# Performance work log

Measured on AMD Instinct MI355X. Metric: run time of the kernel, lower is better.

The kernel has to match this reference:

```python
import jax, jax.numpy as jnp
import numpy as np
import math

NHID = 32
FEAT_SIZE = 32
FEAT_SIZE_LIST = [16, 32, 32, 32]
SEQ_LEN = len(FEAT_SIZE_LIST)   # 4
N_EDGE_LABELS = 3
NLAYERS = 2
N_GRAPHS = 64
FINAL = SEQ_LEN * NHID          # 128


def _pos_enc(max_len, dim):
    pe = np.zeros((max_len, dim), dtype=np.float32)
    pos = np.arange(max_len, dtype=np.float32)[:, None]
    div = np.exp(np.arange(0, dim, 2, dtype=np.float32) * (-math.log(10000.0) / dim))
    pe[:, 0::2] = np.sin(pos * div)
    pe[:, 1::2] = np.cos(pos * div)
    return jnp.asarray(pe)


def _feature_attention(x, wqkv, w1, b1, w2, b2):
    # x: [N, S*NHID] -> attention over the S feature 'tokens' per node
    N, D = x.shape
    S = D // NHID
    xr = x.reshape(N, S, NHID)
    qkv = jnp.einsum('nsf,fh->nsh', xr, wqkv)          # [N,S,3*NHID]
    q, k, v = jnp.split(qkv, 3, axis=-1)
    att = jax.nn.softmax(jnp.einsum('nsh,nth->nst', q, k) / jnp.sqrt(jnp.asarray(NHID, x.dtype)), axis=-1)
    y = jnp.einsum('nst,nth->nsh', att, v)             # [N,S,NHID]
    y = y + (jax.nn.relu(y @ w1 + b1) @ w2 + b2)       # residual FFN
    return y.reshape(N, -1)


def setup_inputs() -> dict:
    key = jax.random.key(0)
    ks = jax.random.split(key, 16)
    N = 100000
    E = 800000
    inp = {
        'x': jax.random.normal(ks[0], (N, 112), dtype=jnp.float32),
        'edge_index0': jax.random.randint(ks[1], (2, E), 0, N),
        'edge_index1': jax.random.randint(ks[2], (2, E), 0, N),
        'edge_index2': jax.random.randint(ks[3], (2, E), 0, N),
        'batch': jnp.sort(jax.random.randint(ks[4], (N,), 0, N_GRAPHS)),
    }
    s = 0.05
    # FeatureLinear encoder (bias-free)
    inp['W_emb'] = jax.random.normal(ks[5], (FEAT_SIZE, NHID), dtype=jnp.float32) * s
    # Per layer: [root, conv0, conv1, conv2] FeatureAttention params, stacked
    A = 1 + N_EDGE_LABELS
    inp['qkv'] = jax.random.normal(ks[6], (NLAYERS, A, NHID, 3 * NHID), dtype=jnp.float32) * s
    inp['ffn_w1'] = jax.random.normal(ks[7], (NLAYERS, A, NHID, NHID), dtype=jnp.float32) * s
    inp['ffn_b1'] = jnp.zeros((NLAYERS, A, NHID), dtype=jnp.float32)
    inp['ffn_w2'] = jax.random.normal(ks[8], (NLAYERS, A, NHID, NHID), dtype=jnp.float32) * s
    inp['ffn_b2'] = jnp.zeros((NLAYERS, A, NHID), dtype=jnp.float32)
    # Heuristic decoder MLP: 128 -> 128 -> 1
    inp['mlp_w1'] = jax.random.normal(ks[9], (FINAL, FINAL), dtype=jnp.float32) * s
    inp['mlp_b1'] = jnp.zeros((FINAL,), dtype=jnp.float32)
    inp['mlp_w2'] = jax.random.normal(ks[10], (FINAL, 1), dtype=jnp.float32) * s
    inp['mlp_b2'] = jnp.zeros((1,), dtype=jnp.float32)
    return inp


def reference(x, edge_index0, edge_index1, edge_index2, batch,
              W_emb, qkv, ffn_w1, ffn_b1, ffn_w2, ffn_b2,
              mlp_w1, mlp_b1, mlp_w2, mlp_b2):
    N = x.shape[0]
    edge_indices = [edge_index0, edge_index1, edge_index2]

    # padding: split by feat_size_list, right-pad each chunk to FEAT_SIZE
    offs = np.cumsum(FEAT_SIZE_LIST)[:-1].tolist()
    chunks = jnp.split(x, offs, axis=1)
    padded = [jnp.pad(c, ((0, 0), (0, FEAT_SIZE - c.shape[1]))) for c in chunks]
    h = jnp.concatenate(padded, axis=1)                       # [N, SEQ_LEN*FEAT_SIZE]

    # sinusoidal positional encoding over the SEQ_LEN feature tokens
    pe = _pos_enc(10, FEAT_SIZE)[:SEQ_LEN]                    # [SEQ_LEN, FEAT_SIZE]
    h = (h.reshape(N, SEQ_LEN, FEAT_SIZE) + pe[None]).reshape(N, -1)

    # FeatureLinear encoder: per-token linear FEAT_SIZE -> NHID
    h = jnp.einsum('nsf,fh->nsh', h.reshape(N, SEQ_LEN, FEAT_SIZE), W_emb).reshape(N, -1)

    # RGNN layers: root attention + per-edge-label attention->scatter-sum
    for l in range(NLAYERS):
        x_out = _feature_attention(h, qkv[l, 0], ffn_w1[l, 0], ffn_b1[l, 0], ffn_w2[l, 0], ffn_b2[l, 0])
        for e in range(N_EDGE_LABELS):
            a = e + 1
            xt = _feature_attention(h, qkv[l, a], ffn_w1[l, a], ffn_b1[l, a], ffn_w2[l, a], ffn_b2[l, a])
            src, dst = edge_indices[e][0], edge_indices[e][1]
            x_out = x_out + jax.ops.segment_sum(xt[src], dst, num_segments=N)
        h = jax.nn.relu(x_out)

    # global mean pool over graphs
    sums = jax.ops.segment_sum(h, batch, num_segments=N_GRAPHS)
    cnts = jax.ops.segment_sum(jnp.ones((N,), h.dtype), batch, num_segments=N_GRAPHS)
    g = sums / jnp.maximum(cnts, 1.0)[:, None]                # [G, FINAL]

    # heuristic decoder
    out = jax.nn.relu(g @ mlp_w1 + mlp_b1) @ mlp_w2 + mlp_b2  # [G, 1]
    return out.squeeze(1)                                     # [G]
```

## Files before the change

kernel.cpp:

```cpp
#include <hip/hip_runtime.h>
#include <hip/hip_bf16.h>
#include <cstdint>
#include <cstddef>


typedef __attribute__((ext_vector_type(8))) short bf16x8;
typedef __attribute__((ext_vector_type(4))) float f32x4;
typedef __attribute__((ext_vector_type(2))) float f32x2;

#if defined(__has_builtin)
#if __has_builtin(__builtin_amdgcn_cvt_pk_fp8_f32) && __has_builtin(__builtin_amdgcn_cvt_pk_f32_fp8)
#define HW_FP8 1
#endif
#if __has_builtin(__builtin_amdgcn_cvt_pk_bf16_f32)
#define HW_PKBF16 1
#endif
#endif

__device__ inline short f2bf(float f) {
    union { float f; unsigned u; } v; v.f = f;
    unsigned r = (v.u + 0x7FFFu + ((v.u >> 16) & 1u)) >> 16;
    return (short)r;
}
__device__ inline float bf2f(unsigned short b) {
    union { unsigned u; float f; } v; v.u = ((unsigned)b) << 16;
    return v.f;
}
#ifdef HW_PKBF16
typedef __attribute__((ext_vector_type(2))) __bf16 bf16x2_t;
__device__ inline unsigned pk2(float a, float b) {
    union { bf16x2_t v; unsigned u; } c;
    c.v = __builtin_amdgcn_cvt_pk_bf16_f32(a, b);
    return c.u;
}
#else
__device__ inline unsigned pk2(float a, float b) {
    unsigned ua = __float_as_uint(a) + 0x8000u;
    unsigned ub = __float_as_uint(b) + 0x8000u;
    return __builtin_amdgcn_perm(ub, ua, 0x07060302u);
}
#endif

#ifndef HW_FP8
__device__ inline unsigned char f2fp8_sw(float f) {
    unsigned s = (__float_as_uint(f) >> 31) & 1u;
    float a = fminf(fabsf(f), 448.f);
    unsigned char bits;
    if (a < 0.015625f) {
        bits = (unsigned char)__float2int_rn(a * 512.f);
    } else {
        int e; float m = frexpf(a, &e);
        int mf = __float2int_rn(m * 16.f);
        if (mf == 16) { mf = 8; e += 1; }
        int ef = e - 1 + 7;
        if (ef > 15) { ef = 15; mf = 14; }
        bits = (unsigned char)((ef << 3) | (mf & 7));
    }
    return (unsigned char)((s << 7) | bits);
}
__device__ inline float fp82f_sw(unsigned b) {
    int s = (b >> 7) & 1, e = (b >> 3) & 15, m = b & 7;
    float v = e ? ldexpf((float)(8 + m), e - 10) : ldexpf((float)m, -9);
    return s ? -v : v;
}
#endif

__device__ inline unsigned pk4fp8(float v0, float v1, float v2, float v3) {
#ifdef HW_FP8
    int w = __builtin_amdgcn_cvt_pk_fp8_f32(v0, v1, 0, false);
    w = __builtin_amdgcn_cvt_pk_fp8_f32(v2, v3, w, true);
    return (unsigned)w;
#else
    return (unsigned)f2fp8_sw(v0) | ((unsigned)f2fp8_sw(v1) << 8) |
           ((unsigned)f2fp8_sw(v2) << 16) | ((unsigned)f2fp8_sw(v3) << 24);
#endif
}
__device__ inline float2 up2fp8(unsigned short raw) {
#ifdef HW_FP8
    f32x2 f = __builtin_amdgcn_cvt_pk_f32_fp8((int)(unsigned)raw, false);
    return make_float2(f[0], f[1]);
#else
    return make_float2(fp82f_sw(raw & 0xffu), fp82f_sw((raw >> 8) & 0xffu));
#endif
}

__device__ inline void acc8(float* a, uint2 v) {
#ifdef HW_FP8
    f32x2 f0 = __builtin_amdgcn_cvt_pk_f32_fp8((int)v.x, false);
    f32x2 f1 = __builtin_amdgcn_cvt_pk_f32_fp8((int)v.x, true);
    f32x2 f2 = __builtin_amdgcn_cvt_pk_f32_fp8((int)v.y, false);
    f32x2 f3 = __builtin_amdgcn_cvt_pk_f32_fp8((int)v.y, true);
    a[0] += f0[0]; a[1] += f0[1]; a[2] += f1[0]; a[3] += f1[1];
    a[4] += f2[0]; a[5] += f2[1]; a[6] += f3[0]; a[7] += f3[1];
#else
    unsigned b0 = v.x, b1 = v.y;
#pragma unroll
    for (int j = 0; j < 4; ++j) a[j]     += fp82f_sw((b0 >> (8 * j)) & 0xffu);
#pragma unroll
    for (int j = 0; j < 4; ++j) a[4 + j] += fp82f_sw((b1 >> (8 * j)) & 0xffu);
#endif
}

__global__ __launch_bounds__(64) void wprep_kernel(
    const float* __restrict__ qkv, const float* __restrict__ fw1,
    const float* __restrict__ fw2, const float* __restrict__ Wemb,
    unsigned short* __restrict__ wpack, float* __restrict__ pwc,
    int* __restrict__ bcnt, int* __restrict__ gres,
    float* __restrict__ gsum, float* __restrict__ gcnt)
{
    const int pi = blockIdx.x;
    const int lane = threadIdx.x;
    const int gid = pi * 64 + lane;
    for (int i = gid; i < 256; i += 512) { bcnt[i] = 0; gres[i] = 0; }
    for (int i = gid; i < 64 * 128; i += 512) gsum[i] = 0.f;
    if (gid < 64) gcnt[gid] = 0.f;

    const int q = lane >> 4, m = lane & 15;
    const float* Wq = qkv + (size_t)pi * 32 * 96;
    const float* W1 = fw1 + (size_t)pi * 32 * 32;
    const float* W2 = fw2 + (size_t)pi * 32 * 32;
    unsigned short* dst = wpack + (size_t)pi * 10 * 64 * 8;
#pragma unroll
    for (int ci = 0; ci < 6; ++ci)
#pragma unroll
        for (int j = 0; j < 8; ++j)
            dst[(ci * 64 + lane) * 8 + j] =
                (unsigned short)f2bf(Wq[(q * 8 + j) * 96 + ci * 16 + m]);
#pragma unroll
    for (int t = 0; t < 2; ++t)
#pragma unroll
        for (int j = 0; j < 8; ++j) {
            dst[((6 + t) * 64 + lane) * 8 + j] =
                (unsigned short)f2bf(W1[(q * 8 + j) * 32 + t * 16 + m]);
            dst[((8 + t) * 64 + lane) * 8 + j] =
                (unsigned short)f2bf(W2[(q * 8 + j) * 32 + t * 16 + m]);
        }

    if (pi == 0) {
        const int c = lane & 31;
        for (int ts = lane >> 5; ts < 4; ts += 2) {
            float accp = 0.f;
            for (int f = 0; f < 32; ++f) {
                float div = __expf(-(float)(f & ~1) * (logf(10000.0f) / 32.0f));
                float ang = (float)ts * div;
                float pv = (f & 1) ? cosf(ang) : sinf(ang);
                accp += pv * Wemb[f * 32 + c];
            }
            pwc[ts * 32 + c] = accp;
        }
    }
}

__global__ __launch_bounds__(256) void enc_kernel(
    const float* __restrict__ x, const float* __restrict__ Wemb,
    const float* __restrict__ pwc, unsigned short* __restrict__ h, int N)
{
    __shared__ float sx[64 * 116];
    const int t = threadIdx.x;
    const int nbase = blockIdx.x * 64;

    {
        const float4* xg = (const float4*)x;
        const size_t g4base = ((size_t)nbase * 112) >> 2;
        const size_t lim4 = ((size_t)N * 112) >> 2;
#pragma unroll
        for (int rep = 0; rep < 7; ++rep) {
            int i = t + rep * 256;
            float4 v = make_float4(0.f, 0.f, 0.f, 0.f);
            if (g4base + (size_t)i < lim4) v = xg[g4base + i];
            int row = i / 28;
            int col4 = i - row * 28;
            *(float4*)&sx[row * 116 + col4 * 4] = v;
        }
    }
    __syncthreads();

    const int nl = t >> 2, ts = t & 3;
    const int node = nbase + nl;
    const int offs_[4] = {0, 16, 48, 80};
    const int nv_[4] = {4, 8, 8, 8};
    const int off = offs_[ts];
    const int nv = nv_[ts];

    float xr[32];
#pragma unroll
    for (int j = 0; j < 8; ++j) {
        float4 v = make_float4(0.f, 0.f, 0.f, 0.f);
        if (j < nv) v = *(const float4*)&sx[nl * 116 + off + 4 * j];
        *(float4*)&xr[4 * j] = v;
    }

    float acc[32];
    {
        const float4* pw4 = (const float4*)(pwc + ts * 32);
#pragma unroll
        for (int j = 0; j < 8; ++j) *(float4*)&acc[4 * j] = pw4[j];
    }

#pragma unroll
    for (int f = 0; f < 32; ++f) {
        float xv = xr[f];
#pragma unroll
        for (int c = 0; c < 32; ++c)
            acc[c] = fmaf(xv, Wemb[f * 32 + c], acc[c]);
    }

    if (node < N) {
        unsigned rp[16];
#pragma unroll
        for (int j = 0; j < 16; ++j) rp[j] = pk2(acc[2 * j], acc[2 * j + 1]);
        unsigned short* hp = h + (size_t)node * 128 + ts * 32;
#pragma unroll
        for (int j = 0; j < 4; ++j)
            ((uint4*)hp)[j] = make_uint4(rp[4 * j], rp[4 * j + 1],
                                         rp[4 * j + 2], rp[4 * j + 3]);
    }
}

#define ATT_WAVES 4
#define WLDS 5376

__global__ __launch_bounds__(256, 3) void attn4_kernel(
    const unsigned short* __restrict__ in,
    unsigned short* __restrict__ outR, unsigned char* __restrict__ out3,
    const unsigned short* __restrict__ wpack,
    const float* __restrict__ fb1, const float* __restrict__ fb2,
    int pibase, int N)
{
    __shared__ char smem[ATT_WAVES * 2 * WLDS];
    const int lane = threadIdx.x & 63;
    const int wave = threadIdx.x >> 6;
    const int q = lane >> 4;
    const int m = lane & 15;

    char* wb0 = smem + wave * (2 * WLDS);

#pragma unroll
    for (int u = 0; u < 2; ++u) {
        int* p32 = (int*)(wb0 + u * WLDS + 4096);
        for (int i = lane; i < 320; i += 64) p32[i] = 0;
    }

    const f32x4 zf = {0.f, 0.f, 0.f, 0.f};
    const int pi = pibase + wave;
    unsigned char* out8 = out3 + (size_t)(wave - 1) * N * 128;

    bf16x8 wqkv[6], w1f[2], w2f[2];
    float b1r[2][4], b2r[2][4];
    {
        const unsigned short* wp = wpack + ((size_t)pi * 10 * 64 + lane) * 8;
#pragma unroll
        for (int ci = 0; ci < 6; ++ci)
            wqkv[ci] = *(const bf16x8*)(wp + ci * 64 * 8);
#pragma unroll
        for (int t = 0; t < 2; ++t) {
            w1f[t] = *(const bf16x8*)(wp + (6 + t) * 64 * 8);
            w2f[t] = *(const bf16x8*)(wp + (8 + t) * 64 * 8);
#pragma unroll
            for (int r = 0; r < 4; ++r) {
                b1r[t][r] = fb1[pi * 32 + 16 * t + q * 4 + r];
                b2r[t][r] = fb2[pi * 32 + 16 * t + q * 4 + r];
            }
        }
    }

    const int nsuper = (N + 7) >> 3;
    for (int stile = blockIdx.x; stile < nsuper; stile += gridDim.x) {
        const int n0 = stile * 8;

        bf16x8 ax[2];
#pragma unroll
        for (int u = 0; u < 2; ++u) {
            bf16x8 a = {0, 0, 0, 0, 0, 0, 0, 0};
            int nm = n0 + 4 * u + (m >> 2);
            if (nm < N)
                a = *(const bf16x8*)(in + (size_t)(n0 + 4 * u) * 128 + m * 32 + q * 8);
            ax[u] = a;
        }

#pragma unroll
        for (int u = 0; u < 2; ++u) {
            char* wbu = wb0 + u * WLDS;
            short* Qb = (short*)(wbu);
            short* Kb = (short*)(wbu + 1280);
            short* VT = (short*)(wbu + 2560);
            short* Pb = (short*)(wbu + 4096);

            f32x4 aQ[2], aK[2], aV[2];
#pragma unroll
            for (int t = 0; t < 2; ++t) {
                aQ[t] = __builtin_amdgcn_mfma_f32_16x16x32_bf16(wqkv[t],     ax[u], zf, 0, 0, 0);
                aK[t] = __builtin_amdgcn_mfma_f32_16x16x32_bf16(wqkv[2 + t], ax[u], zf, 0, 0, 0);
                aV[t] = __builtin_amdgcn_mfma_f32_16x16x32_bf16(ax[u], wqkv[4 + t], zf, 0, 0, 0);
            }
#pragma unroll
            for (int t = 0; t < 2; ++t) {
                uint2 dq, dk, dv;
                dq.x = pk2(aQ[t][0], aQ[t][1]); dq.y = pk2(aQ[t][2], aQ[t][3]);
                dk.x = pk2(aK[t][0], aK[t][1]); dk.y = pk2(aK[t][2], aK[t][3]);
                dv.x = pk2(aV[t][0], aV[t][1]); dv.y = pk2(aV[t][2], aV[t][3]);
                *(uint2*)(Qb + m * 40 + 16 * t + q * 4) = dq;
                *(uint2*)(Kb + m * 40 + 16 * t + q * 4) = dk;
                *(uint2*)(VT + (16 * t + m) * 24 + q * 4) = dv;
            }

            bf16x8 aKf = *(const bf16x8*)(Kb + m * 40 + q * 8);
            bf16x8 bQf = *(const bf16x8*)(Qb + m * 40 + q * 8);
            f32x4 st = __builtin_amdgcn_mfma_f32_16x16x32_bf16(aKf, bQf, zf, 0, 0, 0);

            float v0 = st[0] * 0.1767766952966369f;
            float v1 = st[1] * 0.1767766952966369f;
            float v2 = st[2] * 0.1767766952966369f;
            float v3 = st[3] * 0.1767766952966369f;
            float mx = fmaxf(fmaxf(v0, v1), fmaxf(v2, v3));
            float e0 = __expf(v0 - mx), e1 = __expf(v1 - mx);
            float e2 = __expf(v2 - mx), e3 = __expf(v3 - mx);
            float inv = 1.0f / (e0 + e1 + e2 + e3);
            if (q == (m >> 2)) {
                uint2 dp;
                dp.x = pk2(e0 * inv, e1 * inv);
                dp.y = pk2(e2 * inv, e3 * inv);
                *(uint2*)(Pb + m * 40 + q * 4) = dp;
            }

            f32x4 y[2];
#pragma unroll
            for (int t = 0; t < 2; ++t) {
                bf16x8 aVf = {0, 0, 0, 0, 0, 0, 0, 0};
                bf16x8 bPf = {0, 0, 0, 0, 0, 0, 0, 0};
                if (q < 2) {
                    aVf = *(const bf16x8*)(VT + (16 * t + m) * 24 + q * 8);
                    bPf = *(const bf16x8*)(Pb + m * 40 + q * 8);
                }
                y[t] = __builtin_amdgcn_mfma_f32_16x16x32_bf16(aVf, bPf, zf, 0, 0, 0);
            }
#pragma unroll
            for (int t = 0; t < 2; ++t) {
                uint2 dy;
                dy.x = pk2(y[t][0], y[t][1]); dy.y = pk2(y[t][2], y[t][3]);
                *(uint2*)(Qb + m * 40 + 16 * t + q * 4) = dy;
            }

            bf16x8 bY = *(const bf16x8*)(Qb + m * 40 + q * 8);
            f32x4 z1[2];
#pragma unroll
            for (int t = 0; t < 2; ++t)
                z1[t] = __builtin_amdgcn_mfma_f32_16x16x32_bf16(w1f[t], bY, zf, 0, 0, 0);
#pragma unroll
            for (int t = 0; t < 2; ++t) {
                uint2 dz;
                dz.x = pk2(fmaxf(z1[t][0] + b1r[t][0], 0.f),
                           fmaxf(z1[t][1] + b1r[t][1], 0.f));
                dz.y = pk2(fmaxf(z1[t][2] + b1r[t][2], 0.f),
                           fmaxf(z1[t][3] + b1r[t][3], 0.f));
                *(uint2*)(Kb + m * 40 + 16 * t + q * 4) = dz;
            }

            bf16x8 bZ = *(const bf16x8*)(Kb + m * 40 + q * 8);
            f32x4 o[2];
#pragma unroll
            for (int t = 0; t < 2; ++t)
                o[t] = __builtin_amdgcn_mfma_f32_16x16x32_bf16(w2f[t], bZ, zf, 0, 0, 0);

            if (n0 + 4 * u + (m >> 2) < N) {
                if (wave == 0) {
#pragma unroll
                    for (int t = 0; t < 2; ++t) {
                        uint2 dd;
                        dd.x = pk2(y[t][0] + o[t][0] + b2r[t][0],
                                   y[t][1] + o[t][1] + b2r[t][1]);
                        dd.y = pk2(y[t][2] + o[t][2] + b2r[t][2],
                                   y[t][3] + o[t][3] + b2r[t][3]);
                        *(uint2*)(outR + (size_t)(n0 + 4 * u) * 128 + m * 32 + 16 * t + q * 4) = dd;
                    }
                } else {
#pragma unroll
                    for (int t = 0; t < 2; ++t) {
                        unsigned pw8 = pk4fp8(
                            (y[t][0] + o[t][0] + b2r[t][0]) * 16.f,
                            (y[t][1] + o[t][1] + b2r[t][1]) * 16.f,
                            (y[t][2] + o[t][2] + b2r[t][2]) * 16.f,
                            (y[t][3] + o[t][3] + b2r[t][3]) * 16.f);
                        *(unsigned*)(out8 + (size_t)(n0 + 4 * u) * 128 + m * 32 + 16 * t + q * 4) = pw8;
                    }
                }
            }
        }
    }
}

#define PA_CHUNK 4096
#define PA_SHIFT 9
#define PA_MAXB  256
#define HB_K     16

__global__ __launch_bounds__(256) void histB_kernel(
    const int* __restrict__ e0, const int* __restrict__ e1,
    const int* __restrict__ e2, int* __restrict__ bcnt, int E)
{
    __shared__ int lh[PA_MAXB];
    const int lab = blockIdx.y;
    const int* e = (lab == 0) ? e0 : (lab == 1) ? e1 : e2;
    const int t = threadIdx.x;
    for (int i = t; i < PA_MAXB; i += 256) lh[i] = 0;
    __syncthreads();
    const int base = blockIdx.x * 256 * HB_K;
#pragma unroll
    for (int k = 0; k < HB_K; ++k) {
        int i = base + k * 256 + t;
        if (i < E) atomicAdd(&lh[e[E + i] >> PA_SHIFT], 1);
    }
    __syncthreads();
    for (int i = t; i < PA_MAXB; i += 256)
        if (lh[i]) atomicAdd(&bcnt[i], lh[i]);
}

__global__ __launch_bounds__(256) void bscan_kernel(
    const int* __restrict__ bcnt, int* __restrict__ bbase)
{
    __shared__ int sd[PA_MAXB];
    const int t = threadIdx.x;
    sd[t] = bcnt[t];
    __syncthreads();
    int own = sd[t];
    for (int o = 1; o < 256; o <<= 1) {
        int v = (t >= o) ? sd[t - o] : 0;
        __syncthreads();
        sd[t] += v;
        __syncthreads();
    }
    bbase[t] = sd[t] - own;
}

__global__ __launch_bounds__(256) void placeA_kernel(
    const int* __restrict__ e0, const int* __restrict__ e1, const int* __restrict__ e2,
    const int* __restrict__ bbase, int* __restrict__ gres,
    int2* __restrict__ pairs, int E, int N)
{
    __shared__ int2 sStage[PA_CHUNK];
    __shared__ int sCnt[PA_MAXB], sScan[PA_MAXB], sCur[PA_MAXB], sGB[PA_MAXB];

    const int lab = blockIdx.y;
    const int t = threadIdx.x;
    const int base = blockIdx.x * PA_CHUNK;
    const int* e = (lab == 0) ? e0 : (lab == 1) ? e1 : e2;
    const int srcoff = lab * N;
    const int nbins = (N + (1 << PA_SHIFT) - 1) >> PA_SHIFT;

    for (int i = t; i < PA_MAXB; i += 256) { sCnt[i] = 0; sCur[i] = 0; }
    __syncthreads();

    int msrc[16], mdst[16];
    const int cnt_total = min(PA_CHUNK, E - base);
#pragma unroll
    for (int k = 0; k < 16; ++k) {
        int i = base + k * 256 + t;
        if (i < E) {
            msrc[k] = srcoff + e[i];
            int d = e[E + i];
            mdst[k] = d;
            atomicAdd(&sCnt[d >> PA_SHIFT], 1);
        } else mdst[k] = -1;
    }
    __syncthreads();

    sScan[t] = sCnt[t];
    __syncthreads();
    for (int o = 1; o < 256; o <<= 1) {
        int v = (t >= o) ? sScan[t - o] : 0;
        __syncthreads();
        sScan[t] += v;
        __syncthreads();
    }
    if (t < nbins && sCnt[t] > 0)
        sGB[t] = bbase[t] + atomicAdd(&gres[t], sCnt[t]);
    __syncthreads();

#pragma unroll
    for (int k = 0; k < 16; ++k) {
        if (mdst[k] >= 0) {
            int bin = mdst[k] >> PA_SHIFT;
            int r = atomicAdd(&sCur[bin], 1);
            sStage[(sScan[bin] - sCnt[bin]) + r] = make_int2(msrc[k], mdst[k]);
        }
    }
    __syncthreads();

    for (int i = t; i < cnt_total; i += 256) {
        int2 pr = sStage[i];
        int bin = pr.y >> PA_SHIFT;
        pairs[sGB[bin] + (i - (sScan[bin] - sCnt[bin]))] = pr;
    }
}

__global__ __launch_bounds__(512) void placeB_kernel(
    const int2* __restrict__ pairs, const int* __restrict__ bbase,
    const int* __restrict__ bcnt, int* __restrict__ offs,
    int* __restrict__ csr, int N, int nbins)
{
    __shared__ int sCnt[512], sScan[512], sFill[512];
    const int bin = blockIdx.x;
    const int t = threadIdx.x;
    const int n0 = bin << PA_SHIFT;
    const int n1 = min(n0 + 512, N);
    const int len = n1 - n0;
    const int rb  = bbase[bin];
    const int cnt = bcnt[bin];
    const int2* gp = pairs + rb;

    sCnt[t] = 0; sFill[t] = 0;
    __syncthreads();
    for (int i = t; i < cnt; i += 512)
        atomicAdd(&sCnt[gp[i].y - n0], 1);
    __syncthreads();
    sScan[t] = sCnt[t];
    __syncthreads();
    for (int o = 1; o < 512; o <<= 1) {
        int v = (t >= o) ? sScan[t - o] : 0;
        __syncthreads();
        sScan[t] += v;
        __syncthreads();
    }
    const int excl = sScan[t] - sCnt[t];
    if (t < len) offs[n0 + t] = rb + excl;
    if (bin == nbins - 1 && t == 0) offs[N] = rb + cnt;
    sScan[t] = excl;
    __syncthreads();

    for (int i = t; i < cnt; i += 512) {
        int2 pr = gp[i];
        int ln = pr.y - n0;
        int p = atomicAdd(&sFill[ln], 1);
        csr[rb + sScan[ln] + p] = pr.x;
    }
}

__global__ __launch_bounds__(256) void agg3_kernel(
    const unsigned short* __restrict__ xtR,
    const unsigned char* __restrict__ xt3,
    const int* __restrict__ csr, const int* __restrict__ offs,
    unsigned short* __restrict__ hout, int N)
{
    const int w = threadIdx.x >> 6, lane = threadIdx.x & 63;
    const int dst = blockIdx.x * 4 + w;
    if (dst >= N) return;

    const int g = lane >> 4;
    const unsigned fl8 = (unsigned)(lane & 15) << 3;

    bf16x8 rv = *(const bf16x8*)(xtR + (size_t)dst * 128 + fl8);

    float a[8];
#pragma unroll
    for (int i = 0; i < 8; ++i) a[i] = 0.f;

    const int beg = offs[dst], end = offs[dst + 1];
    if (beg < end) {
        const int last = end - 1;
        int e0 = beg + g, e1 = beg + 4 + g;
        int c0 = csr[min(e0, last)];
        int c1 = csr[min(e1, last)];
        c0 = (e0 > last) ? -1 : c0;
        c1 = (e1 > last) ? -1 : c1;
        for (int k = beg; k < end; k += 8) {
            const int nk = k + 8;
            unsigned s0 = (unsigned)max(c0, 0);
            unsigned s1 = (unsigned)max(c1, 0);
            uint2 v0 = *(const uint2*)(xt3 + (s0 << 7) + fl8);
            uint2 v1 = *(const uint2*)(xt3 + (s1 << 7) + fl8);
            int ne0 = nk + g, ne1 = nk + 4 + g;
            int n0_ = csr[min(ne0, last)];
            int n1_ = csr[min(ne1, last)];
            n0_ = (ne0 > last) ? -1 : n0_;
            n1_ = (ne1 > last) ? -1 : n1_;
            v0.x = (c0 < 0) ? 0u : v0.x;  v0.y = (c0 < 0) ? 0u : v0.y;
            v1.x = (c1 < 0) ? 0u : v1.x;  v1.y = (c1 < 0) ? 0u : v1.y;
            acc8(a, v0);
            acc8(a, v1);
            c0 = n0_; c1 = n1_;
        }
    }

#pragma unroll
    for (int i = 0; i < 8; ++i) {
        a[i] += __shfl_xor(a[i], 16);
        a[i] += __shfl_xor(a[i], 32);
    }

    if (g == 0) {
        unsigned r[4];
#pragma unroll
        for (int t = 0; t < 4; ++t) {
            float f0 = bf2f((unsigned short)rv[2 * t])     + 0.0625f * a[2 * t];
            float f1 = bf2f((unsigned short)rv[2 * t + 1]) + 0.0625f * a[2 * t + 1];
            r[t] = pk2(fmaxf(f0, 0.f), fmaxf(f1, 0.f));
        }
        uint4 st = make_uint4(r[0], r[1], r[2], r[3]);
        *(uint4*)(hout + (size_t)dst * 128 + fl8) = st;
    }
}

__global__ __launch_bounds__(256) void pool_kernel(
    const unsigned short* __restrict__ in, const int* __restrict__ batch,
    float* __restrict__ gsum, float* __restrict__ gcnt, int N)
{
    int t = threadIdx.x;
    int j = t & 127, half = t >> 7;
    int n0 = blockIdx.x * 64 + half * 32;
    float acc = 0.f, c = 0.f; int cur = -1;
    for (int i = 0; i < 32; ++i) {
        int n = n0 + i;
        if (n >= N) break;
        int g = batch[n];
        if (g != cur) {
            if (cur >= 0) {
                atomicAdd(&gsum[cur * 128 + j], acc);
                if (j == 0) atomicAdd(&gcnt[cur], c);
            }
            cur = g; acc = 0.f; c = 0.f;
        }
        acc += bf2f(in[(size_t)n * 128 + j]);
        c += 1.f;
    }
    if (cur >= 0) {
        atomicAdd(&gsum[cur * 128 + j], acc);
        if (j == 0) atomicAdd(&gcnt[cur], c);
    }
}

__global__ __launch_bounds__(128) void dec_kernel(
    const float* __restrict__ gsum, const float* __restrict__ gcnt,
    const float* __restrict__ W1, const float* __restrict__ B1,
    const float* __restrict__ W2, const float* __restrict__ B2,
    float* __restrict__ out)
{
    __shared__ float sg[128];
    __shared__ float sh[128];
    int t = threadIdx.x, b = blockIdx.x;
    float cinv = 1.0f / fmaxf(gcnt[b], 1.0f);
    sg[t] = gsum[b * 128 + t] * cinv;
    __syncthreads();
    float acc = B1[t];
    for (int f = 0; f < 128; ++f) acc += sg[f] * W1[f * 128 + t];
    sh[t] = fmaxf(acc, 0.f) * W2[t];
    __syncthreads();
    for (int o = 64; o > 0; o >>= 1) {
        if (t < o) sh[t] += sh[t + o];
        __syncthreads();
    }
    if (t == 0) out[b] = sh[0] + B2[0];
}

extern "C" void kernel_launch(void* const* d_in, const int* in_sizes, int n_in,
                              void* d_out, int out_size, void* d_ws, size_t ws_size,
                              hipStream_t stream)
{
    const float* x    = (const float*)d_in[0];
    const int*   e0   = (const int*)d_in[1];
    const int*   e1   = (const int*)d_in[2];
    const int*   e2   = (const int*)d_in[3];
    const int*   bat  = (const int*)d_in[4];
    const float* Wemb = (const float*)d_in[5];
    const float* qkv  = (const float*)d_in[6];
    const float* fw1  = (const float*)d_in[7];
    const float* fb1  = (const float*)d_in[8];
    const float* fw2  = (const float*)d_in[9];
    const float* fb2  = (const float*)d_in[10];
    const float* mw1  = (const float*)d_in[11];
    const float* mb1  = (const float*)d_in[12];
    const float* mw2  = (const float*)d_in[13];
    const float* mb2  = (const float*)d_in[14];
    const int N = in_sizes[0] / 112;
    const int E = in_sizes[1] / 2;
    float* outp = (float*)d_out;
    (void)n_in; (void)out_size; (void)ws_size;

    char* w = (char*)d_ws;
    auto alloc = [&](size_t bytes) {
        char* p = w; w += (bytes + 255) & ~(size_t)255; return p;
    };
    unsigned short* h0    = (unsigned short*)alloc((size_t)N * 128 * 2);
    unsigned short* h1    = (unsigned short*)alloc((size_t)N * 128 * 2);
    unsigned short* xtR   = (unsigned short*)alloc((size_t)N * 128 * 2);
    unsigned char*  xt3   = (unsigned char*)alloc((size_t)3 * N * 128);
    unsigned short* wpack = (unsigned short*)alloc(8 * 10 * 64 * 8 * 2);
    float* pwc   = (float*)alloc(128 * 4);
    int*   csr   = (int*)alloc((size_t)3 * E * 4);
    int*   offs  = (int*)alloc((size_t)(N + 1) * 4);
    int*   bcnt  = (int*)alloc(PA_MAXB * 4);
    int*   bbase = (int*)alloc(PA_MAXB * 4);
    int*   gres  = (int*)alloc(PA_MAXB * 4);
    float* gsum  = (float*)alloc(64 * 128 * 4);
    float* gcnt  = (float*)alloc(64 * 4);
    int2* pairs = (int2*)xtR;

    const int nbins = (N + (1 << PA_SHIFT) - 1) >> PA_SHIFT;

    wprep_kernel<<<8, 64, 0, stream>>>(qkv, fw1, fw2, Wemb, wpack, pwc,
                                       bcnt, gres, gsum, gcnt);
    enc_kernel<<<(N + 63) / 64, 256, 0, stream>>>(x, Wemb, pwc, h0, N);

    histB_kernel<<<dim3((E + 256 * HB_K - 1) / (256 * HB_K), 3), 256, 0, stream>>>(
        e0, e1, e2, bcnt, E);
    bscan_kernel<<<1, 256, 0, stream>>>(bcnt, bbase);
    placeA_kernel<<<dim3((E + PA_CHUNK - 1) / PA_CHUNK, 3), 256, 0, stream>>>(
        e0, e1, e2, bbase, gres, pairs, E, N);
    placeB_kernel<<<nbins, 512, 0, stream>>>(pairs, bbase, bcnt, offs, csr, N, nbins);

    const int ATT_GRID = 768;
    auto run_layer = [&](const unsigned short* lin, unsigned short* lout, int l) {
        attn4_kernel<<<ATT_GRID, 256, 0, stream>>>(
            lin, xtR, xt3, wpack, fb1, fb2, l * 4, N);
        agg3_kernel<<<(N + 3) / 4, 256, 0, stream>>>(xtR, xt3, csr, offs, lout, N);
    };
    run_layer(h0, h1, 0);
    run_layer(h1, h0, 1);

    pool_kernel<<<(N + 63) / 64, 256, 0, stream>>>(h0, bat, gsum, gcnt, N);
    dec_kernel<<<64, 128, 0, stream>>>(gsum, gcnt, mw1, mb1, mw2, mb2, outp);
}
```

Measured before the change: 467.6 us.

## Remap aggregation to eight lanes per destination node with zero-row padding

```diff
diff --git a/kernel.cpp b/kernel.cpp
--- a/kernel.cpp
+++ b/kernel.cpp
@@ -100,11 +100,16 @@
     for (int j = 0; j < 4; ++j) a[4 + j] += fp82f_sw((b1 >> (8 * j)) & 0xffu);
 #endif
 }
+__device__ inline void acc16(float* a, uint4 v) {
+    acc8(a,     make_uint2(v.x, v.y));
+    acc8(a + 8, make_uint2(v.z, v.w));
+}
 
 __global__ __launch_bounds__(64) void wprep_kernel(
     const float* __restrict__ qkv, const float* __restrict__ fw1,
     const float* __restrict__ fw2, const float* __restrict__ Wemb,
     unsigned short* __restrict__ wpack, float* __restrict__ pwc,
+    unsigned char* __restrict__ xtzr,
     int* __restrict__ bcnt, int* __restrict__ gres,
     float* __restrict__ gsum, float* __restrict__ gcnt)
 {
@@ -114,6 +119,7 @@
     for (int i = gid; i < 256; i += 512) { bcnt[i] = 0; gres[i] = 0; }
     for (int i = gid; i < 64 * 128; i += 512) gsum[i] = 0.f;
     if (gid < 64) gcnt[gid] = 0.f;
+    if (gid < 32) ((int*)xtzr)[gid] = 0;
 
     const int q = lane >> 4, m = lane & 15;
     const float* Wq = qkv + (size_t)pi * 32 * 96;
@@ -541,62 +547,61 @@
     const int* __restrict__ csr, const int* __restrict__ offs,
     unsigned short* __restrict__ hout, int N)
 {
-    const int w = threadIdx.x >> 6, lane = threadIdx.x & 63;
-    const int dst = blockIdx.x * 4 + w;
-    if (dst >= N) return;
-
-    const int g = lane >> 4;
-    const unsigned fl8 = (unsigned)(lane & 15) << 3;
-
-    bf16x8 rv = *(const bf16x8*)(xtR + (size_t)dst * 128 + fl8);
-
-    float a[8];
-#pragma unroll
-    for (int i = 0; i < 8; ++i) a[i] = 0.f;
-
-    const int beg = offs[dst], end = offs[dst + 1];
-    if (beg < end) {
-        const int last = end - 1;
-        int e0 = beg + g, e1 = beg + 4 + g;
-        int c0 = csr[min(e0, last)];
-        int c1 = csr[min(e1, last)];
-        c0 = (e0 > last) ? -1 : c0;
-        c1 = (e1 > last) ? -1 : c1;
-        for (int k = beg; k < end; k += 8) {
-            const int nk = k + 8;
-            unsigned s0 = (unsigned)max(c0, 0);
-            unsigned s1 = (unsigned)max(c1, 0);
-            uint2 v0 = *(const uint2*)(xt3 + (s0 << 7) + fl8);
-            uint2 v1 = *(const uint2*)(xt3 + (s1 << 7) + fl8);
-            int ne0 = nk + g, ne1 = nk + 4 + g;
-            int n0_ = csr[min(ne0, last)];
-            int n1_ = csr[min(ne1, last)];
-            n0_ = (ne0 > last) ? -1 : n0_;
-            n1_ = (ne1 > last) ? -1 : n1_;
-            v0.x = (c0 < 0) ? 0u : v0.x;  v0.y = (c0 < 0) ? 0u : v0.y;
-            v1.x = (c1 < 0) ? 0u : v1.x;  v1.y = (c1 < 0) ? 0u : v1.y;
-            acc8(a, v0);
-            acc8(a, v1);
-            c0 = n0_; c1 = n1_;
-        }
-    }
-
-#pragma unroll
-    for (int i = 0; i < 8; ++i) {
-        a[i] += __shfl_xor(a[i], 16);
-        a[i] += __shfl_xor(a[i], 32);
-    }
-
-    if (g == 0) {
-        unsigned r[4];
+    const int wv = threadIdx.x >> 6, lane = threadIdx.x & 63;
+    const int oct = lane >> 3;
+    const int fl  = lane & 7;
+    const int dst = blockIdx.x * 32 + wv * 8 + oct;
+    const int ZR  = 3 * N;
+    const unsigned fb = (unsigned)fl << 4;
+
+    const int beg = offs[min(dst, N)];
+    const int end = offs[min(dst + 1, N)];
+    const int last = end - 1;
+
+    const unsigned short* rp = xtR + (size_t)min(dst, N - 1) * 128 + fl * 16;
+    bf16x8 rv0 = *(const bf16x8*)(rp);
+    bf16x8 rv1 = *(const bf16x8*)(rp + 8);
+
+    float a[16];
+#pragma unroll
+    for (int i = 0; i < 16; ++i) a[i] = 0.f;
+
+    int k = beg;
+    int i0 = csr[k];
+    int i1 = csr[k + 1];
+    int c0 = (k     > last) ? ZR : i0;
+    int c1 = (k + 1 > last) ? ZR : i1;
+
+    while (__any(k < end)) {
+        uint4 v0 = *(const uint4*)(xt3 + (((unsigned)c0) << 7) + fb);
+        uint4 v1 = *(const uint4*)(xt3 + (((unsigned)c1) << 7) + fb);
+        int k2 = min(k + 2, end);
+        int j0 = csr[k2];
+        int j1 = csr[k2 + 1];
+        c0 = (k2     > last) ? ZR : j0;
+        c1 = (k2 + 1 > last) ? ZR : j1;
+        acc16(a, v0);
+        acc16(a, v1);
+        k = k2;
+    }
+
+    if (dst < N) {
+        unsigned r[8];
 #pragma unroll
         for (int t = 0; t < 4; ++t) {
-            float f0 = bf2f((unsigned short)rv[2 * t])     + 0.0625f * a[2 * t];
-            float f1 = bf2f((unsigned short)rv[2 * t + 1]) + 0.0625f * a[2 * t + 1];
+            float f0 = bf2f((unsigned short)rv0[2 * t])     + 0.0625f * a[2 * t];
+            float f1 = bf2f((unsigned short)rv0[2 * t + 1]) + 0.0625f * a[2 * t + 1];
             r[t] = pk2(fmaxf(f0, 0.f), fmaxf(f1, 0.f));
         }
-        uint4 st = make_uint4(r[0], r[1], r[2], r[3]);
-        *(uint4*)(hout + (size_t)dst * 128 + fl8) = st;
+#pragma unroll
+        for (int t = 0; t < 4; ++t) {
+            float f0 = bf2f((unsigned short)rv1[2 * t])     + 0.0625f * a[8 + 2 * t];
+            float f1 = bf2f((unsigned short)rv1[2 * t + 1]) + 0.0625f * a[8 + 2 * t + 1];
+            r[4 + t] = pk2(fmaxf(f0, 0.f), fmaxf(f1, 0.f));
+        }
+        unsigned short* hp = hout + (size_t)dst * 128 + fl * 16;
+        *(uint4*)hp       = make_uint4(r[0], r[1], r[2], r[3]);
+        *(uint4*)(hp + 8) = make_uint4(r[4], r[5], r[6], r[7]);
     }
 }
 
@@ -682,10 +687,10 @@
     unsigned short* h0    = (unsigned short*)alloc((size_t)N * 128 * 2);
     unsigned short* h1    = (unsigned short*)alloc((size_t)N * 128 * 2);
     unsigned short* xtR   = (unsigned short*)alloc((size_t)N * 128 * 2);
-    unsigned char*  xt3   = (unsigned char*)alloc((size_t)3 * N * 128);
+    unsigned char*  xt3   = (unsigned char*)alloc((size_t)3 * N * 128 + 128);
     unsigned short* wpack = (unsigned short*)alloc(8 * 10 * 64 * 8 * 2);
     float* pwc   = (float*)alloc(128 * 4);
-    int*   csr   = (int*)alloc((size_t)3 * E * 4);
+    int*   csr   = (int*)alloc((size_t)3 * E * 4 + 64);
     int*   offs  = (int*)alloc((size_t)(N + 1) * 4);
     int*   bcnt  = (int*)alloc(PA_MAXB * 4);
     int*   bbase = (int*)alloc(PA_MAXB * 4);
@@ -693,10 +698,11 @@
     float* gsum  = (float*)alloc(64 * 128 * 4);
     float* gcnt  = (float*)alloc(64 * 4);
     int2* pairs = (int2*)xtR;
+    unsigned char* xtzr = xt3 + (size_t)3 * N * 128;
 
     const int nbins = (N + (1 << PA_SHIFT) - 1) >> PA_SHIFT;
 
-    wprep_kernel<<<8, 64, 0, stream>>>(qkv, fw1, fw2, Wemb, wpack, pwc,
+    wprep_kernel<<<8, 64, 0, stream>>>(qkv, fw1, fw2, Wemb, wpack, pwc, xtzr,
                                        bcnt, gres, gsum, gcnt);
     enc_kernel<<<(N + 63) / 64, 256, 0, stream>>>(x, Wemb, pwc, h0, N);
 
@@ -711,7 +717,7 @@
     auto run_layer = [&](const unsigned short* lin, unsigned short* lout, int l) {
         attn4_kernel<<<ATT_GRID, 256, 0, stream>>>(
             lin, xtR, xt3, wpack, fb1, fb2, l * 4, N);
-        agg3_kernel<<<(N + 3) / 4, 256, 0, stream>>>(xtR, xt3, csr, offs, lout, N);
+        agg3_kernel<<<(N + 31) / 32, 256, 0, stream>>>(xtR, xt3, csr, offs, lout, N);
     };
     run_layer(h0, h1, 0);
     run_layer(h1, h0, 1);
```

New measurement: 465.7 us. No clear change (-0.4%).
